# Kernel optimization log

Measured on AMD Instinct MI355X. Metric: run time of the kernel, lower is better.

## Reference

```python
import jax, jax.numpy as jnp
import numpy as np

EPS = 1e-5  # torch LayerNorm default
H = 8       # heads_num


def _ln(t, g, b):
    m = jnp.mean(t, axis=-1, keepdims=True)
    v = jnp.var(t, axis=-1, keepdims=True)
    return (t - m) / jnp.sqrt(v + EPS) * g + b


def setup_inputs() -> dict:
    key = jax.random.key(0)
    ks = jax.random.split(key, 12)
    B, S, Dq, Dk, Dff = 4, 2048, 512, 768, 2048
    def w(k, shape, scale=0.02):
        return jax.random.normal(k, shape, jnp.float32) * scale
    return {
        "x": jax.random.normal(ks[0], (B, S, Dq), jnp.float32),
        "y": jax.random.normal(ks[1], (B, S, Dk), jnp.float32),
        # cross-attention projections (stored [in, out]; linear_q/k/v have no bias)
        "Wq": w(ks[2], (Dq, Dq)), "Wk": w(ks[3], (Dk, Dq)), "Wv": w(ks[4], (Dk, Dq)),
        "Wo": w(ks[5], (Dq, Dq)), "bo": jnp.zeros((Dq,), jnp.float32),
        # nn.MultiheadAttention packed in-projection and out-projection
        "mha_w_in": w(ks[6], (Dq, 3 * Dq)), "mha_b_in": jnp.zeros((3 * Dq,), jnp.float32),
        "mha_wo": w(ks[7], (Dq, Dq)), "mha_bo": jnp.zeros((Dq,), jnp.float32),
        # 4 LayerNorms
        "ln1_g": jnp.ones((Dq,), jnp.float32), "ln1_b": jnp.zeros((Dq,), jnp.float32),
        "ln2_g": jnp.ones((Dk,), jnp.float32), "ln2_b": jnp.zeros((Dk,), jnp.float32),
        "ln3_g": jnp.ones((Dq,), jnp.float32), "ln3_b": jnp.zeros((Dq,), jnp.float32),
        "ln4_g": jnp.ones((Dq,), jnp.float32), "ln4_b": jnp.zeros((Dq,), jnp.float32),
        # dense MLP (moe=False branch)
        "mlp_w1": w(ks[8], (Dq, Dff)), "mlp_b1": jnp.zeros((Dff,), jnp.float32),
        "mlp_w2": w(ks[9], (Dff, Dq)), "mlp_b2": jnp.zeros((Dq,), jnp.float32),
    }


def reference(x, y, Wq, Wk, Wv, Wo, bo, mha_w_in, mha_b_in, mha_wo, mha_bo,
              ln1_g, ln1_b, ln2_g, ln2_b, ln3_g, ln3_b, ln4_g, ln4_b,
              mlp_w1, mlp_b1, mlp_w2, mlp_b2):
    B, S, D = x.shape
    hd = D // H
    inv_sqrt_hd = 1.0 / np.sqrt(hd).astype(np.float32)

    xn = _ln(x, ln1_g, ln1_b)
    yn = _ln(y, ln2_g, ln2_b)

    # ---- Multi_CrossAttention: manual QK^T softmax V over true seq axis ----
    q = (xn @ Wq).reshape(B, S, H, hd)
    k = (yn @ Wk).reshape(B, -1, H, hd)
    v = (yn @ Wv).reshape(B, -1, H, hd)
    scores = jnp.einsum('bqhd,bkhd->bhqk', q, k) * inv_sqrt_hd  # [B,H,S,S] (512 MB)
    attn = jax.nn.softmax(scores, axis=-1)
    ctx = jnp.einsum('bhqk,bkhd->bqhd', attn, v).reshape(B, S, D)
    ca = ctx @ Wo + bo

    h = _ln(ca + xn, ln3_g, ln3_b)

    # ---- nn.MultiheadAttention (batch_first=False!): axis 0 is the sequence ----
    qkv = h @ mha_w_in + mha_b_in  # [L=B, N=S, 3D]
    q2, k2, v2 = jnp.split(qkv, 3, axis=-1)
    L, N = q2.shape[0], q2.shape[1]
    q2 = q2.reshape(L, N, H, hd)
    k2 = k2.reshape(L, N, H, hd)
    v2 = v2.reshape(L, N, H, hd)
    s2 = jnp.einsum('lnhd,mnhd->nhlm', q2, k2) * inv_sqrt_hd  # [N,H,L,L]
    a2 = jax.nn.softmax(s2, axis=-1)
    sa = jnp.einsum('nhlm,mnhd->lnhd', a2, v2).reshape(L, N, D) @ mha_wo + mha_bo

    h2 = _ln(sa + h, ln4_g, ln4_b)

    # ---- dense MLP (GELU exact, dropout=0) ----
    mlp = jax.nn.gelu(h2 @ mlp_w1 + mlp_b1, approximate=False) @ mlp_w2 + mlp_b2
    return mlp + h2
```

## Files before the change

### kernel.cpp

```cpp
#include <hip/hip_runtime.h>
#include <math.h>

typedef unsigned short u16;
typedef __attribute__((ext_vector_type(8))) short bf8;
typedef __attribute__((ext_vector_type(4))) float f4;
typedef __attribute__((ext_vector_type(4))) unsigned int u32x4;
typedef __attribute__((ext_vector_type(2))) unsigned int u32x2;
typedef __attribute__((ext_vector_type(4))) unsigned short u16x4;
typedef __attribute__((ext_vector_type(8))) unsigned short u16x8;

__device__ __forceinline__ float bf2f(u16 a){
  unsigned u = ((unsigned)a) << 16;
  float f; __builtin_memcpy(&f, &u, 4);
  return f;
}
__device__ __forceinline__ u16 f2bf(float f){
  unsigned u; __builtin_memcpy(&u, &f, 4);
  u += 0x7fffu + ((u >> 16) & 1u);
  return (u16)(u >> 16);
}
__device__ __forceinline__ unsigned packbf(float a, float b){
  unsigned ua, ub;
  __builtin_memcpy(&ua, &a, 4); __builtin_memcpy(&ub, &b, 4);
  ua += 0x8000u; ub += 0x8000u;
  return __builtin_amdgcn_perm(ub, ua, 0x07060302u);
}
__device__ __forceinline__ void gload16(const u16* g, u16* l){
  __builtin_amdgcn_global_load_lds((const __attribute__((address_space(1))) void*)g,
                                   (__attribute__((address_space(3))) void*)l, 16, 0, 0);
}
__device__ __forceinline__ int xcd_swizzle(int orig, int nwg){
  const int qq = nwg >> 3, rr = nwg & 7;
  const int xcd = orig & 7, loc = orig >> 3;
  return (xcd < rr ? xcd * (qq + 1) : rr * (qq + 1) + (xcd - rr) * qq) + loc;
}

__global__ void k_transpose_all(
    const float* __restrict__ Wq, const float* __restrict__ Wk,
    const float* __restrict__ Wv, const float* __restrict__ Wo,
    const float* __restrict__ Win, const float* __restrict__ Wmo,
    const float* __restrict__ W1, const float* __restrict__ W2,
    u16* __restrict__ WqT, u16* __restrict__ WkT, u16* __restrict__ WvT,
    u16* __restrict__ WoT, u16* __restrict__ WinT, u16* __restrict__ WmoT,
    u16* __restrict__ W1T, u16* __restrict__ W2T)
{
  __shared__ float tile[32][33];
  const int tid = blockIdx.x;
  const float* in; u16* out; int R, C, lo;
  if (tid < 1280){
    if (tid < 256)       { in = Wq;  out = WqT;  R = 512; C = 512;  lo = 0; }
    else if (tid < 640)  { in = Wk;  out = WkT;  R = 768; C = 512;  lo = 256; }
    else if (tid < 1024) { in = Wv;  out = WvT;  R = 768; C = 512;  lo = 640; }
    else                 { in = Wo;  out = WoT;  R = 512; C = 512;  lo = 1024; }
  } else {
    if (tid < 2048)      { in = Win; out = WinT; R = 512; C = 1536; lo = 1280; }
    else if (tid < 2304) { in = Wmo; out = WmoT; R = 512; C = 512;  lo = 2048; }
    else if (tid < 3328) { in = W1;  out = W1T;  R = 512; C = 2048; lo = 2304; }
    else                 { in = W2;  out = W2T;  R = 2048; C = 512; lo = 3328; }
  }
  const int local = tid - lo;
  const int tpx = C >> 5;
  const int bx = (local % tpx) * 32, by = (local / tpx) * 32;
  const int tx = threadIdx.x, ty = threadIdx.y;
#pragma unroll
  for (int i = 0; i < 4; i++)
    tile[ty + i*8][tx] = in[(size_t)(by + ty + i*8) * C + bx + tx];
  __syncthreads();
#pragma unroll
  for (int i = 0; i < 4; i++)
    out[(size_t)(bx + ty + i*8) * R + by + tx] = f2bf(tile[tx][ty + i*8]);
}

__device__ __forceinline__ void ln_row(
    const float* __restrict__ r, const float* __restrict__ gam,
    const float* __restrict__ bet, float* __restrict__ outf,
    u16* __restrict__ outb, int D, int t)
{
  const int nv = D >> 8;
  float v[3] = {0.f, 0.f, 0.f};
  float s = 0.f, s2 = 0.f;
#pragma unroll
  for (int i = 0; i < 3; i++){
    if (i < nv){ float xx = r[t + i*256]; v[i] = xx; s += xx; s2 += xx*xx; }
  }
#pragma unroll
  for (int m = 32; m; m >>= 1){ s += __shfl_xor(s, m); s2 += __shfl_xor(s2, m); }
  __shared__ float rs[4], rq[4];
  const int wave = t >> 6;
  if ((t & 63) == 0){ rs[wave] = s; rq[wave] = s2; }
  __syncthreads();
  s  = rs[0] + rs[1] + rs[2] + rs[3];
  s2 = rq[0] + rq[1] + rq[2] + rq[3];
  const float mean = s / (float)D;
  const float var  = s2 / (float)D - mean * mean;
  const float rstd = rsqrtf(var + 1e-5f);
#pragma unroll
  for (int i = 0; i < 3; i++){
    if (i < nv){
      const int c = t + i*256;
      float o = (v[i] - mean) * rstd * gam[c] + bet[c];
      if (outf) outf[c] = o;
      outb[c] = f2bf(o);
    }
  }
}

__global__ __launch_bounds__(256) void k_layernorm(
    const float* __restrict__ in, const float* __restrict__ gam,
    const float* __restrict__ bet, float* __restrict__ outf,
    u16* __restrict__ outb, int D)
{
  const int row = blockIdx.x;
  ln_row(in + (size_t)row * D, gam, bet,
         outf ? outf + (size_t)row * D : nullptr,
         outb + (size_t)row * D, D, threadIdx.x);
}

__global__ __launch_bounds__(256) void k_layernorm12(
    const float* __restrict__ x, const float* __restrict__ y,
    const float* __restrict__ g1, const float* __restrict__ b1,
    const float* __restrict__ g2, const float* __restrict__ b2,
    float* __restrict__ xnF, u16* __restrict__ xnB, u16* __restrict__ ynB)
{
  const int row = blockIdx.x;
  if (row < 8192){
    ln_row(x + (size_t)row * 512, g1, b1, xnF + (size_t)row * 512,
           xnB + (size_t)row * 512, 512, threadIdx.x);
  } else {
    const int r2 = row - 8192;
    ln_row(y + (size_t)r2 * 768, g2, b2, nullptr,
           ynB + (size_t)r2 * 768, 768, threadIdx.x);
  }
}

template<int TM, int TN, bool BIAS, bool RES, bool GELU_ACT, int OUTM>
__global__ __launch_bounds__(256, 4) void k_gemm(
    const u16* __restrict__ A, const u16* __restrict__ BT,
    const float* __restrict__ bias, const float* __restrict__ res,
    float* __restrict__ outf, u16* __restrict__ outb,
    int M, int N, int K)
{
  constexpr int MF = TM / 32;
  constexpr int NF = TN / 32;
  constexpr int WM = TM / 2;
  constexpr int WN = TN / 2;
  __shared__ u16 Sb[(TM + TN) * 64];
  const int t = threadIdx.x;
  const int gx = gridDim.x;
  const int swz = xcd_swizzle(blockIdx.y * gx + blockIdx.x, gx * gridDim.y);
  const int m0 = (swz / gx) * TM, n0 = (swz % gx) * TN;
  const int wave = t >> 6, lane = t & 63;
  const int wm = wave >> 1, wn = wave & 1;
  const int l15 = lane & 15, lg = lane >> 4;
  const u16* Ag = A + (size_t)m0 * K;
  const u16* Bg = BT + (size_t)n0 * K;

  const int lrow = lane >> 3;
  const int csrc = (((lane & 7) ^ lrow) << 3);
  const u16* Agl = Ag + (size_t)lrow * K + csrc;
  const u16* Bgl = Bg + (size_t)lrow * K + csrc;

  f4 acc[MF][NF];
#pragma unroll
  for (int i = 0; i < MF; i++)
#pragma unroll
    for (int j = 0; j < NF; j++) acc[i][j] = (f4){0.f, 0.f, 0.f, 0.f};

  const int nK = K >> 6;
#pragma unroll
  for (int i = 0; i < TM/32; i++){
    const int rb = (i*4 + wave) * 8;
    gload16(Agl + (size_t)rb * K, &Sb[rb * 64]);
  }
#pragma unroll
  for (int i = 0; i < TN/32; i++){
    const int rb = (i*4 + wave) * 8;
    gload16(Bgl + (size_t)rb * K, &Sb[(TM + rb) * 64]);
  }
  asm volatile("s_waitcnt vmcnt(0)" ::: "memory");
  __syncthreads();

  for (int kt = 0;; kt++){
    const char* As = (const char*)&Sb[0];
    const char* Bs = (const char*)&Sb[TM * 64];
#pragma unroll
    for (int kc = 0; kc < 2; kc++){
      bf8 af[MF], bfr[NF];
      const int kb = kc*64 + lg*16;
#pragma unroll
      for (int mf = 0; mf < MF; mf++){
        const int row = wm*WM + mf*16 + l15;
        af[mf] = *(const bf8*)(As + row*128 + (kb ^ ((row & 7) << 4)));
      }
#pragma unroll
      for (int nf = 0; nf < NF; nf++){
        const int row = wn*WN + nf*16 + l15;
        bfr[nf] = *(const bf8*)(Bs + row*128 + (kb ^ ((row & 7) << 4)));
      }
#pragma unroll
      for (int mf = 0; mf < MF; mf++)
#pragma unroll
        for (int nf = 0; nf < NF; nf++)
          acc[mf][nf] = __builtin_amdgcn_mfma_f32_16x16x32_bf16(af[mf], bfr[nf], acc[mf][nf], 0, 0, 0);
    }
    if (kt + 1 == nK) break;
    __syncthreads();
    const int ko = (kt + 1) << 6;
#pragma unroll
    for (int i = 0; i < TM/32; i++){
      const int rb = (i*4 + wave) * 8;
      gload16(Agl + (size_t)rb * K + ko, &Sb[rb * 64]);
    }
#pragma unroll
    for (int i = 0; i < TN/32; i++){
      const int rb = (i*4 + wave) * 8;
      gload16(Bgl + (size_t)rb * K + ko, &Sb[(TM + rb) * 64]);
    }
    asm volatile("s_waitcnt vmcnt(0)" ::: "memory");
    __syncthreads();
  }
#pragma unroll
  for (int mf = 0; mf < MF; mf++){
#pragma unroll
    for (int nf = 0; nf < NF; nf++){
      const int colg = n0 + wn*WN + nf*16 + l15;
      const int rowg = m0 + wm*WM + mf*16 + lg*4;
      const float bv = BIAS ? bias[colg] : 0.f;
      float vv[4];
#pragma unroll
      for (int j = 0; j < 4; j++){
        float v = acc[mf][nf][j] + bv;
        if (RES) v += res[(size_t)(rowg + j) * N + colg];
        if (GELU_ACT) v = 0.5f * v * (1.f + erff(v * 0.7071067811865475f));
        vv[j] = v;
      }
      if (OUTM == 0){
#pragma unroll
        for (int j = 0; j < 4; j++) outf[(size_t)(rowg + j) * N + colg] = vv[j];
      } else if (OUTM == 1){
#pragma unroll
        for (int j = 0; j < 4; j++) outb[(size_t)(rowg + j) * N + colg] = f2bf(vv[j]);
      } else {
        const int bb = rowg >> 11, ss = rowg & 2047;
        u16x4 pk;
#pragma unroll
        for (int j = 0; j < 4; j++) pk[j] = f2bf(vv[j]);
        *(u16x4*)(outb + ((size_t)(bb*512 + colg)) * 2048 + ss) = pk;
      }
    }
  }
}

__global__ __launch_bounds__(256, 4) void k_flash(
    const u16* __restrict__ q, const u16* __restrict__ k,
    const u16* __restrict__ vt, u16* __restrict__ ctx)
{
  __shared__ char Kb[2][64 * 128];
  __shared__ char Vb[2][64 * 128];
  __shared__ char Pb[4][16 * 128];
  const int t = threadIdx.x;
  const int wave = t >> 6, lane = t & 63;
  const int l15 = lane & 15, lg = lane >> 4;
  const int id = blockIdx.y * 32 + blockIdx.x;
  const int swz = xcd_swizzle(id, 1024);
  const int qb = swz & 31, bh = swz >> 5;
  const int b = bh >> 3, h = bh & 7;
  const int qrow0 = qb*64 + wave*16;
  constexpr float CEXP = 0.125f * 1.44269504f;

  const u16* qp = q + ((size_t)(b*2048 + qrow0 + l15)) * 512 + h*64 + lg*8;
  const bf8 qf0 = *(const bf8*)qp;
  const bf8 qf1 = *(const bf8*)(qp + 32);

  const int srow = t >> 3;
  const int sw0  = srow*128 + ((((t & 7) << 4)) ^ ((srow & 7) << 4));
  const u16* kg = k  + ((size_t)(b*2048 + srow)) * 512  + h*64 + ((t & 7) << 3);
  const u16* vg = vt + ((size_t)(b*512 + h*64 + srow)) * 2048 + ((t & 7) << 3);

  u32x4 rk0 = *(const u32x4*)kg;
  u32x4 rk1 = *(const u32x4*)(kg + 32*512);
  u32x4 rv0 = *(const u32x4*)vg;
  u32x4 rv1 = *(const u32x4*)(vg + 32*2048);
  *(u32x4*)(Kb[0] + sw0)          = rk0;
  *(u32x4*)(Kb[0] + sw0 + 32*128) = rk1;
  *(u32x4*)(Vb[0] + sw0)          = rv0;
  *(u32x4*)(Vb[0] + sw0 + 32*128) = rv1;

  f4 o[4];
#pragma unroll
  for (int nb = 0; nb < 4; nb++) o[nb] = (f4){0.f,0.f,0.f,0.f};
  float rl = 0.f;
  char* myp = Pb[wave];
  const int psw = (l15 & 7) << 4;

  int cur = 0;
  for (int it = 0; it < 32; it++){
    __syncthreads();
    if (it + 1 < 32){
      const size_t kt = (size_t)(it + 1) << 6;
      rk0 = *(const u32x4*)(kg + kt*512);
      rk1 = *(const u32x4*)(kg + kt*512 + 32*512);
      rv0 = *(const u32x4*)(vg + kt);
      rv1 = *(const u32x4*)(vg + kt + 32*2048);
    }
    const char* kbuf = Kb[cur];
    const char* vbuf = Vb[cur];
    f4 s[4];
    __builtin_amdgcn_s_setprio(1);
#pragma unroll
    for (int nb = 0; nb < 4; nb++){
      const int row = nb*16 + l15;
      const int sx = (row & 7) << 4;
      const bf8 kf0 = *(const bf8*)(kbuf + row*128 + ((lg*16) ^ sx));
      const bf8 kf1 = *(const bf8*)(kbuf + row*128 + ((64 + lg*16) ^ sx));
      f4 a = (f4){0.f,0.f,0.f,0.f};
      a = __builtin_amdgcn_mfma_f32_16x16x32_bf16(kf0, qf0, a, 0, 0, 0);
      a = __builtin_amdgcn_mfma_f32_16x16x32_bf16(kf1, qf1, a, 0, 0, 0);
      s[nb] = a;
    }
    __builtin_amdgcn_s_setprio(0);
    float p[4][4];
#pragma unroll
    for (int nb = 0; nb < 4; nb++)
#pragma unroll
      for (int j = 0; j < 4; j++)
        p[nb][j] = __builtin_amdgcn_exp2f(s[nb][j] * CEXP);
    float ts = ((p[0][0]+p[1][0]) + (p[2][0]+p[3][0]))
             + ((p[0][1]+p[1][1]) + (p[2][1]+p[3][1]))
             + ((p[0][2]+p[1][2]) + (p[2][2]+p[3][2]))
             + ((p[0][3]+p[1][3]) + (p[2][3]+p[3][3]));
    ts += __shfl_xor(ts, 16);
    ts += __shfl_xor(ts, 32);
    rl += ts;
#pragma unroll
    for (int nb = 0; nb < 4; nb++){
      u32x2 w;
      w[0] = packbf(p[nb][0], p[nb][1]);
      w[1] = packbf(p[nb][2], p[nb][3]);
      *(u32x2*)(myp + l15*128 + ((nb*32 + lg*8) ^ psw)) = w;
    }
    asm volatile("s_waitcnt lgkmcnt(0)" ::: "memory");
    __builtin_amdgcn_sched_barrier(0);
    const bf8 pf0 = *(const bf8*)(myp + l15*128 + ((lg*16) ^ psw));
    const bf8 pf1 = *(const bf8*)(myp + l15*128 + ((64 + lg*16) ^ psw));
    bf8 vf[4][2];
#pragma unroll
    for (int nb = 0; nb < 4; nb++){
      const int row = nb*16 + l15;
      const int sx = (row & 7) << 4;
      vf[nb][0] = *(const bf8*)(vbuf + row*128 + ((lg*16) ^ sx));
      vf[nb][1] = *(const bf8*)(vbuf + row*128 + ((64 + lg*16) ^ sx));
    }
    __builtin_amdgcn_s_setprio(1);
#pragma unroll
    for (int nb = 0; nb < 4; nb++){
      o[nb] = __builtin_amdgcn_mfma_f32_16x16x32_bf16(pf0, vf[nb][0], o[nb], 0, 0, 0);
      o[nb] = __builtin_amdgcn_mfma_f32_16x16x32_bf16(pf1, vf[nb][1], o[nb], 0, 0, 0);
    }
    __builtin_amdgcn_s_setprio(0);
    __syncthreads();
    if (it + 1 < 32){
      char* kb2 = Kb[cur ^ 1];
      char* vb2 = Vb[cur ^ 1];
      *(u32x4*)(kb2 + sw0)          = rk0;
      *(u32x4*)(kb2 + sw0 + 32*128) = rk1;
      *(u32x4*)(vb2 + sw0)          = rv0;
      *(u32x4*)(vb2 + sw0 + 32*128) = rv1;
      cur ^= 1;
    }
  }
  const float i0 = 1.f / __shfl(rl, lg*4 + 0);
  const float i1 = 1.f / __shfl(rl, lg*4 + 1);
  const float i2 = 1.f / __shfl(rl, lg*4 + 2);
  const float i3 = 1.f / __shfl(rl, lg*4 + 3);
#pragma unroll
  for (int nb = 0; nb < 4; nb++){
    u16* cp = ctx + ((size_t)(b*2048 + qrow0 + lg*4)) * 512 + h*64 + nb*16 + l15;
    cp[0]    = f2bf(o[nb][0] * i0);
    cp[512]  = f2bf(o[nb][1] * i1);
    cp[1024] = f2bf(o[nb][2] * i2);
    cp[1536] = f2bf(o[nb][3] * i3);
  }
}

__global__ __launch_bounds__(256) void k_mha_small(const u16* __restrict__ qkv,
                                                   u16* __restrict__ outb)
{
  const int tid = blockIdx.x * 256 + threadIdx.x;
  const int n = tid & 2047;
  const int hl = tid >> 11;
  const int h = hl >> 2, l = hl & 3;
  const u16* qp = qkv + ((size_t)l * 2048 + n) * 1536 + h*64;
  float qv[64];
#pragma unroll
  for (int i = 0; i < 8; i++){
    const bf8 c = *(const bf8*)(qp + i*8);
#pragma unroll
    for (int j2 = 0; j2 < 8; j2++) qv[i*8 + j2] = bf2f((u16)c[j2]) * 0.125f;
  }
  float sc[4];
#pragma unroll
  for (int m = 0; m < 4; m++){
    const u16* kp = qkv + ((size_t)m * 2048 + n) * 1536 + 512 + h*64;
    float a = 0.f;
#pragma unroll
    for (int i = 0; i < 8; i++){
      const bf8 c = *(const bf8*)(kp + i*8);
#pragma unroll
      for (int j2 = 0; j2 < 8; j2++) a += qv[i*8 + j2] * bf2f((u16)c[j2]);
    }
    sc[m] = a;
  }
  const float mx = fmaxf(fmaxf(sc[0], sc[1]), fmaxf(sc[2], sc[3]));
  float p[4]; float sum = 0.f;
#pragma unroll
  for (int m = 0; m < 4; m++){ p[m] = __expf(sc[m] - mx); sum += p[m]; }
  const float inv = 1.f / sum;
  float ov[64];
#pragma unroll
  for (int i = 0; i < 64; i++) ov[i] = 0.f;
#pragma unroll
  for (int m = 0; m < 4; m++){
    const float pw = p[m] * inv;
    const u16* vp = qkv + ((size_t)m * 2048 + n) * 1536 + 1024 + h*64;
#pragma unroll
    for (int i = 0; i < 8; i++){
      const bf8 c = *(const bf8*)(vp + i*8);
#pragma unroll
      for (int j2 = 0; j2 < 8; j2++) ov[i*8 + j2] += pw * bf2f((u16)c[j2]);
    }
  }
  u16* op = outb + ((size_t)l * 2048 + n) * 512 + h*64;
#pragma unroll
  for (int i = 0; i < 8; i++){
    u16x8 pk;
#pragma unroll
    for (int j2 = 0; j2 < 8; j2++) pk[j2] = f2bf(ov[i*8 + j2]);
    *(u16x8*)(op + i*8) = pk;
  }
}

extern "C" void kernel_launch(void* const* d_in, const int* in_sizes, int n_in,
                              void* d_out, int out_size, void* d_ws, size_t ws_size,
                              hipStream_t stream)
{
  (void)in_sizes; (void)n_in; (void)out_size; (void)ws_size;
  const float* x    = (const float*)d_in[0];
  const float* y    = (const float*)d_in[1];
  const float* Wq   = (const float*)d_in[2];
  const float* Wk   = (const float*)d_in[3];
  const float* Wv   = (const float*)d_in[4];
  const float* Wo   = (const float*)d_in[5];
  const float* bo   = (const float*)d_in[6];
  const float* Win  = (const float*)d_in[7];
  const float* bin  = (const float*)d_in[8];
  const float* Wmo  = (const float*)d_in[9];
  const float* bmo  = (const float*)d_in[10];
  const float* ln1g = (const float*)d_in[11];
  const float* ln1b = (const float*)d_in[12];
  const float* ln2g = (const float*)d_in[13];
  const float* ln2b = (const float*)d_in[14];
  const float* ln3g = (const float*)d_in[15];
  const float* ln3b = (const float*)d_in[16];
  const float* ln4g = (const float*)d_in[17];
  const float* ln4b = (const float*)d_in[18];
  const float* W1   = (const float*)d_in[19];
  const float* b1   = (const float*)d_in[20];
  const float* W2   = (const float*)d_in[21];
  const float* b2   = (const float*)d_in[22];

  char* ws = (char*)d_ws;
  const size_t MB = 1024 * 1024;
  u16* WqT  = (u16*)ws;
  u16* WkT  = WqT  + 512 * 512;
  u16* WvT  = WkT  + 512 * 768;
  u16* WoT  = WvT  + 512 * 768;
  u16* WinT = WoT  + 512 * 512;
  u16* WmoT = WinT + 1536 * 512;
  u16* W1T  = WmoT + 512 * 512;
  u16* W2T  = W1T  + 2048 * 512;
  float* hF   = (float*)(ws + 9 * MB);
  float* xnF  = (float*)(ws + 25 * MB);
  float* carF = (float*)(ws + 41 * MB);
  u16* xnB  = (u16*)(ws + 57 * MB);
  u16* ynB  = (u16*)(ws + 65 * MB);
  u16* qB   = (u16*)(ws + 77 * MB);
  u16* kB   = (u16*)(ws + 85 * MB);
  u16* vtB  = (u16*)(ws + 93 * MB);
  u16* ctxB = (u16*)(ws + 101 * MB);
  float* sarF = xnF;
  float* h2F  = carF;
  u16* saB   = xnB;
  u16* hB    = ynB;
  u16* h2B   = qB;
  u16* qkvB  = kB;
  u16* t1B   = (u16*)hF;

  k_transpose_all<<<4352, dim3(32, 8), 0, stream>>>(
      Wq, Wk, Wv, Wo, Win, Wmo, W1, W2,
      WqT, WkT, WvT, WoT, WinT, WmoT, W1T, W2T);

  k_layernorm12<<<16384, 256, 0, stream>>>(x, y, ln1g, ln1b, ln2g, ln2b,
                                           xnF, xnB, ynB);

  k_gemm<64,128,false,false,false,1><<<dim3(4, 128), 256, 0, stream>>>(xnB, WqT, nullptr, nullptr, nullptr, qB,  8192, 512, 512);
  k_gemm<64,128,false,false,false,1><<<dim3(4, 128), 256, 0, stream>>>(ynB, WkT, nullptr, nullptr, nullptr, kB,  8192, 512, 768);
  k_gemm<64,128,false,false,false,2><<<dim3(4, 128), 256, 0, stream>>>(ynB, WvT, nullptr, nullptr, nullptr, vtB, 8192, 512, 768);

  k_flash<<<dim3(32, 32), 256, 0, stream>>>(qB, kB, vtB, ctxB);

  k_gemm<64,128,true,true,false,0><<<dim3(4, 128), 256, 0, stream>>>(ctxB, WoT, bo, xnF, carF, nullptr, 8192, 512, 512);
  k_layernorm<<<8192, 256, 0, stream>>>(carF, ln3g, ln3b, hF, hB, 512);

  k_gemm<128,128,true,false,false,1><<<dim3(12, 64), 256, 0, stream>>>(hB, WinT, bin, nullptr, nullptr, qkvB, 8192, 1536, 512);
  k_mha_small<<<256, 256, 0, stream>>>(qkvB, saB);
  k_gemm<64,128,true,true,false,0><<<dim3(4, 128), 256, 0, stream>>>(saB, WmoT, bmo, hF, sarF, nullptr, 8192, 512, 512);
  k_layernorm<<<8192, 256, 0, stream>>>(sarF, ln4g, ln4b, h2F, h2B, 512);

  k_gemm<128,128,true,false,true,1><<<dim3(16, 64), 256, 0, stream>>>(h2B, W1T, b1, nullptr, nullptr, t1B, 8192, 2048, 512);
  k_gemm<64,128,true,true,false,0><<<dim3(4, 128), 256, 0, stream>>>(t1B, W2T, b2, h2F, (float*)d_out, nullptr, 8192, 512, 2048);
}
```

Baseline: 247.0 us.

## Stream flash K/V tiles directly to LDS and fuse K/V projections

The flash-attention kernel now loads K and V tiles straight from global memory into LDS with gload16 instead of staging them through registers. The XOR swizzle moves to the source column, and the second barrier per iteration is replaced by a vmcnt wait before the first one. Separately, the K and V projection GEMMs become a single launch with N=1024, using a new output mode that writes row-major K for the first half and transposed V for the second. This relies on WkT and WvT sitting next to each other in memory, and the direct-to-LDS path makes each iteration wait on the outstanding loads for the next tile.

```diff
diff --git a/kernel.cpp b/kernel.cpp
--- a/kernel.cpp
+++ b/kernel.cpp
@@ -137,7 +137,7 @@
 __global__ __launch_bounds__(256, 4) void k_gemm(
     const u16* __restrict__ A, const u16* __restrict__ BT,
     const float* __restrict__ bias, const float* __restrict__ res,
-    float* __restrict__ outf, u16* __restrict__ outb,
+    float* __restrict__ outf, u16* __restrict__ outb, u16* __restrict__ outb2,
     int M, int N, int K)
 {
   constexpr int MF = TM / 32;
@@ -240,12 +240,23 @@
       } else if (OUTM == 1){
 #pragma unroll
         for (int j = 0; j < 4; j++) outb[(size_t)(rowg + j) * N + colg] = f2bf(vv[j]);
-      } else {
+      } else if (OUTM == 2){
         const int bb = rowg >> 11, ss = rowg & 2047;
         u16x4 pk;
 #pragma unroll
         for (int j = 0; j < 4; j++) pk[j] = f2bf(vv[j]);
         *(u16x4*)(outb + ((size_t)(bb*512 + colg)) * 2048 + ss) = pk;
+      } else {
+        if (n0 < 512){
+#pragma unroll
+          for (int j = 0; j < 4; j++) outb[(size_t)(rowg + j) * 512 + colg] = f2bf(vv[j]);
+        } else {
+          const int bb = rowg >> 11, ss = rowg & 2047;
+          u16x4 pk;
+#pragma unroll
+          for (int j = 0; j < 4; j++) pk[j] = f2bf(vv[j]);
+          *(u16x4*)(outb2 + ((size_t)(bb*512 + (colg - 512))) * 2048 + ss) = pk;
+        }
       }
     }
   }
@@ -255,8 +266,8 @@
     const u16* __restrict__ q, const u16* __restrict__ k,
     const u16* __restrict__ vt, u16* __restrict__ ctx)
 {
-  __shared__ char Kb[2][64 * 128];
-  __shared__ char Vb[2][64 * 128];
+  __shared__ u16 Kb[2][64 * 64];
+  __shared__ u16 Vb[2][64 * 64];
   __shared__ char Pb[4][16 * 128];
   const int t = threadIdx.x;
   const int wave = t >> 6, lane = t & 63;
@@ -272,19 +283,17 @@
   const bf8 qf0 = *(const bf8*)qp;
   const bf8 qf1 = *(const bf8*)(qp + 32);
 
-  const int srow = t >> 3;
-  const int sw0  = srow*128 + ((((t & 7) << 4)) ^ ((srow & 7) << 4));
-  const u16* kg = k  + ((size_t)(b*2048 + srow)) * 512  + h*64 + ((t & 7) << 3);
-  const u16* vg = vt + ((size_t)(b*512 + h*64 + srow)) * 2048 + ((t & 7) << 3);
-
-  u32x4 rk0 = *(const u32x4*)kg;
-  u32x4 rk1 = *(const u32x4*)(kg + 32*512);
-  u32x4 rv0 = *(const u32x4*)vg;
-  u32x4 rv1 = *(const u32x4*)(vg + 32*2048);
-  *(u32x4*)(Kb[0] + sw0)          = rk0;
-  *(u32x4*)(Kb[0] + sw0 + 32*128) = rk1;
-  *(u32x4*)(Vb[0] + sw0)          = rv0;
-  *(u32x4*)(Vb[0] + sw0 + 32*128) = rv1;
+  const int lrow = lane >> 3;
+  const int csrc = (((lane & 7) ^ lrow) << 3);
+  const u16* kgl = k  + ((size_t)(b*2048 + lrow)) * 512  + h*64 + csrc;
+  const u16* vgl = vt + ((size_t)(b*512 + h*64 + lrow)) * 2048 + csrc;
+
+#pragma unroll
+  for (int i = 0; i < 2; i++){
+    const int rb = (i*4 + wave) * 8;
+    gload16(kgl + (size_t)rb * 512,  &Kb[0][rb * 64]);
+    gload16(vgl + (size_t)rb * 2048, &Vb[0][rb * 64]);
+  }
 
   f4 o[4];
 #pragma unroll
@@ -295,16 +304,19 @@
 
   int cur = 0;
   for (int it = 0; it < 32; it++){
+    asm volatile("s_waitcnt vmcnt(0)" ::: "memory");
     __syncthreads();
     if (it + 1 < 32){
-      const size_t kt = (size_t)(it + 1) << 6;
-      rk0 = *(const u32x4*)(kg + kt*512);
-      rk1 = *(const u32x4*)(kg + kt*512 + 32*512);
-      rv0 = *(const u32x4*)(vg + kt);
-      rv1 = *(const u32x4*)(vg + kt + 32*2048);
-    }
-    const char* kbuf = Kb[cur];
-    const char* vbuf = Vb[cur];
+      const int kt = (it + 1) << 6;
+#pragma unroll
+      for (int i = 0; i < 2; i++){
+        const int rb = (i*4 + wave) * 8;
+        gload16(kgl + (size_t)(kt + rb) * 512,  &Kb[cur^1][rb * 64]);
+        gload16(vgl + (size_t)rb * 2048 + kt,   &Vb[cur^1][rb * 64]);
+      }
+    }
+    const char* kbuf = (const char*)Kb[cur];
+    const char* vbuf = (const char*)Vb[cur];
     f4 s[4];
     __builtin_amdgcn_s_setprio(1);
 #pragma unroll
@@ -358,16 +370,7 @@
       o[nb] = __builtin_amdgcn_mfma_f32_16x16x32_bf16(pf1, vf[nb][1], o[nb], 0, 0, 0);
     }
     __builtin_amdgcn_s_setprio(0);
-    __syncthreads();
-    if (it + 1 < 32){
-      char* kb2 = Kb[cur ^ 1];
-      char* vb2 = Vb[cur ^ 1];
-      *(u32x4*)(kb2 + sw0)          = rk0;
-      *(u32x4*)(kb2 + sw0 + 32*128) = rk1;
-      *(u32x4*)(vb2 + sw0)          = rv0;
-      *(u32x4*)(vb2 + sw0 + 32*128) = rv1;
-      cur ^= 1;
-    }
+    cur ^= 1;
   }
   const float i0 = 1.f / __shfl(rl, lg*4 + 0);
   const float i1 = 1.f / __shfl(rl, lg*4 + 1);
@@ -503,20 +506,19 @@
   k_layernorm12<<<16384, 256, 0, stream>>>(x, y, ln1g, ln1b, ln2g, ln2b,
                                            xnF, xnB, ynB);
 
-  k_gemm<64,128,false,false,false,1><<<dim3(4, 128), 256, 0, stream>>>(xnB, WqT, nullptr, nullptr, nullptr, qB,  8192, 512, 512);
-  k_gemm<64,128,false,false,false,1><<<dim3(4, 128), 256, 0, stream>>>(ynB, WkT, nullptr, nullptr, nullptr, kB,  8192, 512, 768);
-  k_gemm<64,128,false,false,false,2><<<dim3(4, 128), 256, 0, stream>>>(ynB, WvT, nullptr, nullptr, nullptr, vtB, 8192, 512, 768);
+  k_gemm<64,128,false,false,false,1><<<dim3(4, 128), 256, 0, stream>>>(xnB, WqT, nullptr, nullptr, nullptr, qB, nullptr, 8192, 512, 512);
+  k_gemm<64,128,false,false,false,3><<<dim3(8, 128), 256, 0, stream>>>(ynB, WkT, nullptr, nullptr, nullptr, kB, vtB,   8192, 1024, 768);
 
   k_flash<<<dim3(32, 32), 256, 0, stream>>>(qB, kB, vtB, ctxB);
 
-  k_gemm<64,128,true,true,false,0><<<dim3(4, 128), 256, 0, stream>>>(ctxB, WoT, bo, xnF, carF, nullptr, 8192, 512, 512);
+  k_gemm<64,128,true,true,false,0><<<dim3(4, 128), 256, 0, stream>>>(ctxB, WoT, bo, xnF, carF, nullptr, nullptr, 8192, 512, 512);
   k_layernorm<<<8192, 256, 0, stream>>>(carF, ln3g, ln3b, hF, hB, 512);
 
-  k_gemm<128,128,true,false,false,1><<<dim3(12, 64), 256, 0, stream>>>(hB, WinT, bin, nullptr, nullptr, qkvB, 8192, 1536, 512);
+  k_gemm<128,128,true,false,false,1><<<dim3(12, 64), 256, 0, stream>>>(hB, WinT, bin, nullptr, nullptr, qkvB, nullptr, 8192, 1536, 512);
   k_mha_small<<<256, 256, 0, stream>>>(qkvB, saB);
-  k_gemm<64,128,true,true,false,0><<<dim3(4, 128), 256, 0, stream>>>(saB, WmoT, bmo, hF, sarF, nullptr, 8192, 512, 512);
+  k_gemm<64,128,true,true,false,0><<<dim3(4, 128), 256, 0, stream>>>(saB, WmoT, bmo, hF, sarF, nullptr, nullptr, 8192, 512, 512);
   k_layernorm<<<8192, 256, 0, stream>>>(sarF, ln4g, ln4b, h2F, h2B, 512);
 
-  k_gemm<128,128,true,false,true,1><<<dim3(16, 64), 256, 0, stream>>>(h2B, W1T, b1, nullptr, nullptr, t1B, 8192, 2048, 512);
-  k_gemm<64,128,true,true,false,0><<<dim3(4, 128), 256, 0, stream>>>(t1B, W2T, b2, h2F, (float*)d_out, nullptr, 8192, 512, 2048);
-}
+  k_gemm<128,128,true,false,true,1><<<dim3(16, 64), 256, 0, stream>>>(h2B, W1T, b1, nullptr, nullptr, t1B, nullptr, 8192, 2048, 512);
+  k_gemm<64,128,true,true,false,0><<<dim3(4, 128), 256, 0, stream>>>(t1B, W2T, b2, h2F, (float*)d_out, nullptr, nullptr, 8192, 512, 2048);
+}
```

Measured after the change: 242.1 us. 2.0% less time.
